# Performance work log

Measured on AMD Instinct MI355X. Metric: run time of the kernel, lower is better.

The kernel has to match this reference:

```python
import jax, jax.numpy as jnp
import numpy as np

N = 50000          # site nodes
L = 32             # max URL token length
E = 64             # embed_size
H = 128            # hidden_size
E_SIM = 800000     # edges per relation in blocks
E_SUB = 200000     # 'sim' edges classified at the end
NEG = 0.01         # LeakyReLU negative slope

def leaky(x):
    return jnp.where(x >= 0, x, NEG * x)

def lstm_final(x, mask, Wih, Whh, b, reverse):
    # x: [N, L, E], mask: [N, L] bool. Returns packed-sequence final hidden [N, E].
    if reverse:
        x = x[:, ::-1, :]
        mask = mask[:, ::-1]
    h0 = jnp.zeros((x.shape[0], Whh.shape[1]), x.dtype)
    def step(carry, inp):
        h, c = carry
        xt, mt = inp
        g = xt @ Wih.T + h @ Whh.T + b
        i, f, gg, o = jnp.split(g, 4, axis=-1)  # PyTorch gate order i,f,g,o
        cn = jax.nn.sigmoid(f) * c + jax.nn.sigmoid(i) * jnp.tanh(gg)
        hn = jax.nn.sigmoid(o) * jnp.tanh(cn)
        m = mt[:, None]
        return (jnp.where(m, hn, h), jnp.where(m, cn, c)), None
    (h, _), _ = jax.lax.scan(step, (h0, h0), (x.transpose(1, 0, 2), mask.T))
    return h

def graph_conv(h, src, dst, W, b):
    # DGL GraphConv, norm='both': D_dst^{-1/2} A D_src^{-1/2} h W + b  (degrees clamped to >=1)
    n = h.shape[0]
    ones = jnp.ones(src.shape[0], h.dtype)
    out_deg = jnp.clip(jax.ops.segment_sum(ones, src, num_segments=n), 1.0)
    in_deg = jnp.clip(jax.ops.segment_sum(ones, dst, num_segments=n), 1.0)
    feat = h * jax.lax.rsqrt(out_deg)[:, None]
    if W.shape[0] > W.shape[1]:
        feat = feat @ W  # project before gather/scatter when in_dim > out_dim (as DGL does)
        rst = jax.ops.segment_sum(feat[src], dst, num_segments=n)
    else:
        rst = jax.ops.segment_sum(feat[src], dst, num_segments=n) @ W
    return rst * jax.lax.rsqrt(in_deg)[:, None] + b

def setup_inputs():
    key = jax.random.key(0)
    ks = iter(jax.random.split(key, 64))
    def nrm(shape, scale=0.05):
        return jax.random.normal(next(ks), shape, dtype=jnp.float32) * scale
    inp = {}
    inp["inputs_s"] = jax.random.randint(next(ks), (N, L), 0, 128)
    lengths = jax.random.randint(next(ks), (N,), 1, L + 1)
    inp["inputs_sm"] = (jnp.arange(L)[None, :] < lengths[:, None]).astype(jnp.int32)
    inp["inputs_c"] = jax.random.randint(next(ks), (N, 1), 0, 101)
    inp["inputs_co"] = jax.random.randint(next(ks), (N, 1), 0, 92)
    inp["inputs_sl"] = jax.random.randint(next(ks), (N, 1), 0, 6)
    for name, m in [("sim_src", E_SIM), ("sim_dst", E_SIM), ("user_src", E_SIM),
                    ("user_dst", E_SIM), ("esub_src", E_SUB), ("esub_dst", E_SUB)]:
        inp[name] = jax.random.randint(next(ks), (m,), 0, N)
    inp["emb_url"] = nrm((128, E)); inp["emb_cat"] = nrm((101, E))
    inp["emb_country"] = nrm((92, E)); inp["emb_sl"] = nrm((6, E))
    for d in ("f", "b"):
        inp["Wih_" + d] = nrm((4 * E, E)); inp["Whh_" + d] = nrm((4 * E, E))
        inp["b_" + d] = nrm((4 * E,))  # b_ih + b_hh folded into one bias
    inp["fc_W"] = nrm((E, 2 * E)); inp["fc_b"] = nrm((E,))
    for i, din in enumerate([4 * E, H]):
        for rel in ("sim", "user"):
            inp["gcn%d_%s_W" % (i, rel)] = nrm((din, H))
            inp["gcn%d_%s_b" % (i, rel)] = nrm((H,))
    inp["cls_W1"] = nrm((H, 2 * H)); inp["cls_b1"] = nrm((H,))
    inp["bn_g"] = jnp.ones((H,), jnp.float32); inp["bn_b"] = jnp.zeros((H,), jnp.float32)
    inp["cls_W2"] = nrm((2, H)); inp["cls_b2"] = nrm((2,))
    return inp

def reference(inputs_s, inputs_sm, inputs_c, inputs_co, inputs_sl,
              sim_src, sim_dst, user_src, user_dst, esub_src, esub_dst,
              emb_url, emb_cat, emb_country, emb_sl,
              Wih_f, Whh_f, b_f, Wih_b, Whh_b, b_b, fc_W, fc_b,
              gcn0_sim_W, gcn0_sim_b, gcn0_user_W, gcn0_user_b,
              gcn1_sim_W, gcn1_sim_b, gcn1_user_W, gcn1_user_b,
              cls_W1, cls_b1, bn_g, bn_b, cls_W2, cls_b2):
    mask = inputs_sm.astype(bool)
    x = emb_url[inputs_s]                                # [N, L, E]
    hf = lstm_final(x, mask, Wih_f, Whh_f, b_f, False)   # h_n[0]
    hb = lstm_final(x, mask, Wih_b, Whh_b, b_b, True)    # h_n[1]
    h_url = leaky(jnp.concatenate([hf, hb], -1) @ fc_W.T + fc_b)  # dropout = identity (eval)
    h = jnp.concatenate([h_url, emb_cat[inputs_c[:, 0]],
                         emb_country[inputs_co[:, 0]], emb_sl[inputs_sl[:, 0]]], -1)  # [N, 4E]
    layers = [(gcn0_sim_W, gcn0_sim_b, gcn0_user_W, gcn0_user_b),
              (gcn1_sim_W, gcn1_sim_b, gcn1_user_W, gcn1_user_b)]
    for Ws, bs, Wu, bu in layers:  # HeteroGraphConv aggregate='sum'
        h = leaky(graph_conv(h, sim_src, sim_dst, Ws, bs)
                  + graph_conv(h, user_src, user_dst, Wu, bu))
    feat = jnp.concatenate([h[esub_src], h[esub_dst]], -1)  # [E_SUB, 2H]
    z = feat @ cls_W1.T + cls_b1
    z = (z - z.mean(0)) * jax.lax.rsqrt(z.var(0) + 1e-5) * bn_g + bn_b  # BatchNorm1d (batch stats)
    z = jnp.maximum(z, 0.0)
    return z @ cls_W2.T + cls_b2
```

## Files before the change

### kernel.cpp

```cpp
#include <hip/hip_runtime.h>
#include <hip/hip_bf16.h>
#include <stdint.h>

#define N_NODES 50000
#define SEQ_L   32
#define NE_BIG  800000
#define NE_SUB  200000
#define DSTRIDE 64

typedef __hip_bfloat16 bf16;
typedef unsigned short u16;
typedef _Float16 f16;
typedef _Float16 v8h __attribute__((ext_vector_type(8)));
typedef float v4f __attribute__((ext_vector_type(4)));

__device__ __forceinline__ float b2f(bf16 x) { return __bfloat162float(x); }
__device__ __forceinline__ float leakyf(float v) { return v >= 0.f ? v : 0.01f * v; }
__device__ __forceinline__ u16 f2h_bits(float x) { f16 h = (f16)x; u16 b; __builtin_memcpy(&b, &h, 2); return b; }
__device__ __forceinline__ float h2f(u16 b) { f16 h; __builtin_memcpy(&h, &b, 2); return (float)h; }
__device__ __forceinline__ uint pack2h(float a, float b) { return (uint)f2h_bits(a) | ((uint)f2h_bits(b) << 16); }

__device__ __forceinline__ float ldf(const void* p, int i, int isbf) {
  return isbf ? b2f(((const bf16*)p)[i]) : ((const float*)p)[i];
}

__device__ __forceinline__ int detect_isbf(const u16* __restrict__ u) {
  __shared__ int insane;
  if (threadIdx.x == 0) insane = 0;
  __syncthreads();
  int expo = (u[threadIdx.x * 2] >> 7) & 0xFF;
  if (expo >= 147) atomicAdd(&insane, 1);
  __syncthreads();
  return insane == 0;
}

struct PrepArgs {
  const void* Whh_f; const void* Whh_b; const void* fc_W; const void* cls_W1;
  const void* g0sW; const void* g0uW; const void* g1sW; const void* g1uW;
  const void* emb_cat; const void* emb_country; const void* emb_sl;
  const void* fc_b; const void* cls_b1; const void* g0sb; const void* g0ub;
  const void* g1sb; const void* g1ub; const void* bn_g; const void* bn_b;
  const void* cls_W2; const void* cls_b2;
  const void* emb_url; const void* Wih_f; const void* b_f; const void* Wih_b; const void* b_b;
  f16* Whh_h; u16* Bfc; u16* BW1; u16* Bg0; u16* Bg1;
  u16* embc_h; u16* embco_h; u16* embs_h;
  float* fcb; float* b1; float* g0sbP; float* g0ubP; float* g1sbP; float* g1ubP;
  float* bngP; float* bnbP; float* W2P; float* b2P;
  int* cnt4; int* cnt33; int* cur33; float* bnsums; int* dflag;
  float* Xperm;
};

__global__ __launch_bounds__(256) void prep_mega_kernel(PrepArgs A) {
  const int b = blockIdx.x;
  const int t = threadIdx.x;
  const int isbf = detect_isbf((const u16*)A.emb_url);
  auto cpy = [&](const void* s, float* d, int n, int boff) {
    int i = (b - boff) * 256 + t;
    if (i < n) d[i] = ldf(s, i, isbf);
  };
  auto cvh = [&](const void* s, u16* d, int n, int boff) {
    int i = (b - boff) * 256 + t;
    if (i < n) d[i] = f2h_bits(ldf(s, i, isbf));
  };
  auto trh = [&](const void* s, u16* d, int R, int C, int KOFF, int boff) {
    int i = (b - boff) * 256 + t;
    if (i < R * C) { int r = i / C, c = i % C; d[c * 256 + KOFF + r] = f2h_bits(ldf(s, i, isbf)); }
  };
  if      (b <   64) cvh(A.Whh_f, (u16*)A.Whh_h, 16384, 0);
  else if (b <  128) cvh(A.Whh_b, (u16*)(A.Whh_h + 16384), 16384, 64);
  else if (b <  160) cvh(A.fc_W, A.Bfc, 8192, 128);
  else if (b <  288) cvh(A.cls_W1, A.BW1, 32768, 160);
  else if (b <  416) trh(A.g0sW, A.Bg0, 256, 128, 0, 288);
  else if (b <  544) trh(A.g0uW, A.Bg0 + 128 * 256, 256, 128, 0, 416);
  else if (b <  608) trh(A.g1sW, A.Bg1, 128, 128, 0, 544);
  else if (b <  672) trh(A.g1uW, A.Bg1, 128, 128, 128, 608);
  else if (b <  698) cvh(A.emb_cat, A.embc_h, 6464, 672);
  else if (b <  721) cvh(A.emb_country, A.embco_h, 5888, 698);
  else if (b <  723) cvh(A.emb_sl, A.embs_h, 384, 721);
  else if (b <  724) cpy(A.fc_b, A.fcb, 64, 723);
  else if (b <  725) cpy(A.cls_b1, A.b1, 128, 724);
  else if (b <  726) cpy(A.g0sb, A.g0sbP, 128, 725);
  else if (b <  727) cpy(A.g0ub, A.g0ubP, 128, 726);
  else if (b <  728) cpy(A.g1sb, A.g1sbP, 128, 727);
  else if (b <  729) cpy(A.g1ub, A.g1ubP, 128, 728);
  else if (b <  730) cpy(A.bn_g, A.bngP, 128, 729);
  else if (b <  731) cpy(A.bn_b, A.bnbP, 128, 730);
  else if (b <  732) cpy(A.cls_W2, A.W2P, 256, 731);
  else if (b <  733) cpy(A.cls_b2, A.b2P, 2, 732);
  else if (b < 1515) {
    int i = (b - 733) * 256 + t;
    if (i < 4 * N_NODES) A.cnt4[i] = 0;
  } else if (b < 1516) {
    if (t < 64) { A.cnt33[t] = 0; A.cur33[t] = 0; }
    A.bnsums[t] = 0.f;
    if (t == 0) A.dflag[0] = isbf;
  } else {
    int bb = b - 1516;
    int dir = bb >> 7;
    int v = bb & 127;
    const void* Wih = dir ? A.Wih_b : A.Wih_f;
    const void* bias = dir ? A.b_b : A.b_f;
    __shared__ float embL[64];
    if (t < 64) embL[t] = ldf(A.emb_url, v * 64 + t, isbf);
    __syncthreads();
    float acc = ldf(bias, t, isbf);
#pragma unroll 8
    for (int j = 0; j < 64; ++j) acc += embL[j] * ldf(Wih, t * 64 + j, isbf);
    int g = t >> 6, unit = t & 63;
    A.Xperm[(size_t)dir * 128 * 256 + v * 256 + unit * 4 + g] = acc;
  }
}
#define PREP_BLOCKS 1772

__global__ __launch_bounds__(256) void graph_build_kernel(
    const int* __restrict__ sm, int* __restrict__ lens, int* __restrict__ cnt33,
    const int* __restrict__ s0, const int* __restrict__ d0,
    const int* __restrict__ s1, const int* __restrict__ d1,
    int* __restrict__ cnt4, int* __restrict__ col0, int* __restrict__ col1)
{
  const int b = blockIdx.x, t = threadIdx.x;
  const int NBL = (N_NODES + 255) / 256;
  const int NBE = (NE_BIG + 255) / 256;
  if (b < NBL) {
    int i = b * 256 + t;
    if (i >= N_NODES) return;
    int len = 0;
#pragma unroll
    for (int tt = 0; tt < SEQ_L; ++tt) len += sm[i * SEQ_L + tt];
    lens[i] = len;
    atomicAdd(&cnt33[len], 1);
  } else {
    int rel = (b - NBL) / NBE;
    int e = ((b - NBL) % NBE) * 256 + t;
    if (e >= NE_BIG) return;
    const int* s = rel ? s1 : s0;
    const int* d = rel ? d1 : d0;
    int* col = rel ? col1 : col0;
    int* base = cnt4 + (size_t)rel * 2 * N_NODES;
    int sv = s[e], dv = d[e];
    atomicAdd(&base[sv], 1);
    int p = atomicAdd(&base[N_NODES + dv], 1);
    if (p < DSTRIDE) col[(size_t)dv * DSTRIDE + p] = sv;
  }
}
#define GB_BLOCKS (196 + 2 * 3125)

__global__ __launch_bounds__(256) void permfill_rsq_kernel(
    const int* __restrict__ lens, const int* __restrict__ cnt33, int* __restrict__ cur33,
    int* __restrict__ perm,
    const int* __restrict__ cnt4, float* __restrict__ rsq4)
{
  const int b = blockIdx.x, t = threadIdx.x;
  const int NBL = (N_NODES + 255) / 256;
  if (b < NBL) {
    int i = b * 256 + t;
    if (i >= N_NODES) return;
    int len = lens[i];
    int base = 0;
    for (int l = len + 1; l <= SEQ_L; ++l) base += cnt33[l];
    int p = atomicAdd(&cur33[len], 1);
    perm[base + p] = i;
  } else {
    int i = (b - NBL) * 256 + t;
    if (i >= 4 * N_NODES) return;
    int c = cnt4[i]; if (c < 1) c = 1;
    rsq4[i] = __builtin_amdgcn_rsqf((float)c);
  }
}
#define PR_BLOCKS (196 + 782)

__global__ __launch_bounds__(256, 3) void lstm_mfma_kernel(
    const int* __restrict__ perm, const int* __restrict__ lens,
    const int* __restrict__ toksg,
    const float* __restrict__ Xperm,
    const f16* __restrict__ Whh_h,
    u16* __restrict__ hcat_h,
    int nnodes)
{
  __shared__ __align__(16) f16 H[2][64 * 72];
  __shared__ int toksL[2][64];
  __shared__ int permL[64];
  __shared__ int lensL[64];
  __shared__ int smax;
  const int tid = threadIdx.x;
  const int w = tid >> 6;
  const int lane = tid & 63;
  const int quad = lane >> 4;
  const int lid = lane & 15;
  const int dir = blockIdx.y;

  if (tid < 64) {
    int gid = blockIdx.x * 64 + tid;
    int node = -1, len = 0;
    if (gid < nnodes) { node = perm[gid]; len = lens[node]; }
    permL[tid] = node; lensL[tid] = len;
  }
  if (tid == 0) smax = 0;
  for (int i = tid; i < 64 * 72; i += 256) { H[0][i] = (f16)0.f; H[1][i] = (f16)0.f; }
  __syncthreads();
  if (tid < 64 && lensL[tid] > 0) atomicMax(&smax, lensL[tid]);
  __syncthreads();
  const int tmax = smax;

  const f16* Wd = Whh_h + (size_t)dir * 256 * 64;
  v8h Bf[4][2];
#pragma unroll
  for (int g = 0; g < 4; ++g)
#pragma unroll
    for (int kf = 0; kf < 2; ++kf)
      Bf[g][kf] = *(const v8h*)(Wd + (g * 64 + w * 16 + lid) * 64 + kf * 32 + quad * 8);

  int lenv[16];
#pragma unroll
  for (int mt = 0; mt < 4; ++mt)
#pragma unroll
    for (int r = 0; r < 4; ++r) lenv[mt * 4 + r] = lensL[mt * 16 + quad * 4 + r];

  float creg[16];
  f16 hreg[16];
#pragma unroll
  for (int i = 0; i < 16; ++i) { creg[i] = 0.f; hreg[i] = (f16)0.f; }

  const float* Xp = Xperm + (size_t)dir * 128 * 256;

  if (tid < 64) {
    int len = lensL[tid];
    int tok = 0;
    if (len > 0) tok = toksg[(size_t)permL[tid] * SEQ_L + (dir ? (len - 1) : 0)];
    toksL[0][tid] = tok;
  }
  __syncthreads();

  for (int step = 0; step < tmax; ++step) {
    const int rb = step & 1, wb = rb ^ 1;
#pragma unroll
    for (int mt = 0; mt < 4; ++mt) {
      float4 xr[4];
#pragma unroll
      for (int r = 0; r < 4; ++r) {
        int nd = mt * 16 + quad * 4 + r;
        xr[r] = *(const float4*)(Xp + (size_t)toksL[rb][nd] * 256 + (w * 16 + lid) * 4);
      }
      const f16* hb = &H[rb][0];
      int arow = (mt * 16 + lid) * 72 + quad * 8;
      v8h a0 = *(const v8h*)(hb + arow);
      v8h a1 = *(const v8h*)(hb + arow + 32);
      v4f acc[4];
#pragma unroll
      for (int g = 0; g < 4; ++g) {
        v4f a = {0.f, 0.f, 0.f, 0.f};
        a = __builtin_amdgcn_mfma_f32_16x16x32_f16(a0, Bf[g][0], a, 0, 0, 0);
        a = __builtin_amdgcn_mfma_f32_16x16x32_f16(a1, Bf[g][1], a, 0, 0, 0);
        acc[g] = a;
      }
#pragma unroll
      for (int r = 0; r < 4; ++r) {
        int idx = mt * 4 + r;
        int nd = mt * 16 + quad * 4 + r;
        bool act = step < lenv[idx];
        float gi = acc[0][r] + xr[r].x;
        float gf = acc[1][r] + xr[r].y;
        float gG = acc[2][r] + xr[r].z;
        float go = acc[3][r] + xr[r].w;
        float A = __expf(-gi);
        float B = __expf(-gf);
        float C = __expf(-go);
        float D = __expf(2.f * fminf(gG, 15.f));
        float sf = __builtin_amdgcn_rcpf(1.f + B);
        float sitg = (D - 1.f) * __builtin_amdgcn_rcpf((1.f + A) * (D + 1.f));
        float cn = sf * creg[idx] + sitg;
        float E = __expf(2.f * fminf(cn, 15.f));
        float hn = (E - 1.f) * __builtin_amdgcn_rcpf((1.f + C) * (E + 1.f));
        if (act) { creg[idx] = cn; hreg[idx] = (f16)hn; }
        H[wb][nd * 72 + w * 16 + lid] = hreg[idx];
      }
    }
    if (tid < 64 && step + 1 < tmax) {
      int len = lensL[tid];
      int tok = 0;
      if (step + 1 < len) {
        int t = dir ? (len - 2 - step) : (step + 1);
        tok = toksg[(size_t)permL[tid] * SEQ_L + t];
      }
      toksL[wb][tid] = tok;
    }
    __syncthreads();
  }
#pragma unroll
  for (int mt = 0; mt < 4; ++mt)
#pragma unroll
    for (int r = 0; r < 4; ++r) {
      int nd = mt * 16 + quad * 4 + r;
      int gnode = permL[nd];
      if (gnode >= 0) {
        u16 bits; f16 hv = hreg[mt * 4 + r]; __builtin_memcpy(&bits, &hv, 2);
        hcat_h[(size_t)gnode * 128 + dir * 64 + w * 16 + lid] = bits;
      }
    }
}

template<int K, int COLS, int AMODE, bool LEAKY, int OHS, bool EMB, bool BNS>
__global__ __launch_bounds__(256) void mfma_gemm(
    const u16* __restrict__ Ah,
    const int* __restrict__ esrc, const int* __restrict__ edst, const u16* __restrict__ Fh,
    const u16* __restrict__ B,
    const float* __restrict__ bias, const float* __restrict__ bias2,
    const float* __restrict__ rs0, const float* __restrict__ rs1,
    u16* __restrict__ outh0, u16* __restrict__ outh1,
    const int* __restrict__ ic, const int* __restrict__ ico, const int* __restrict__ isl,
    const u16* __restrict__ ech, const u16* __restrict__ ecoh, const u16* __restrict__ eslh,
    float* __restrict__ bnsums,
    int nrows)
{
  constexpr int AST = K + 8;
  constexpr int ABYTES = 64 * AST * 2;
  constexpr int EBYTES = 64 * 129 * 4;
  constexpr int SBYTES = (ABYTES > EBYTES) ? ABYTES : EBYTES;
  __shared__ __align__(16) char smem[SBYTES];
  u16* As = (u16*)smem;
  float* Es = (float*)smem;
  __shared__ int idxL[128];
  __shared__ float bnred[BNS ? 512 : 1];

  const int tid = threadIdx.x;
  const int w = tid >> 6;
  const int lane = tid & 63;
  const int quad = lane >> 4;
  const int lid = lane & 15;
  const int r0 = blockIdx.x * 64;

  if (AMODE == 2) {
    if (tid < 64) {
      int row = r0 + tid;
      idxL[tid] = (row < nrows) ? esrc[row] : -1;
      idxL[64 + tid] = (row < nrows) ? edst[row] : -1;
    }
    __syncthreads();
    for (int idx = tid; idx < 64 * (K / 8); idx += 256) {
      int rn = idx / (K / 8), seg = idx % (K / 8);
      int half = seg >> 4, k8 = seg & 15;
      int base = idxL[half * 64 + rn];
      uint4 v = {0u, 0u, 0u, 0u};
      if (base >= 0) v = *(const uint4*)(Fh + (size_t)base * 128 + k8 * 8);
      *(uint4*)(As + rn * AST + seg * 8) = v;
    }
  } else {
    for (int idx = tid; idx < 64 * (K / 8); idx += 256) {
      int rn = idx / (K / 8), c8 = idx % (K / 8);
      int row = r0 + rn;
      uint4 v = {0u, 0u, 0u, 0u};
      if (row < nrows) v = *(const uint4*)(Ah + (size_t)row * K + c8 * 8);
      *(uint4*)(As + rn * AST + c8 * 8) = v;
    }
  }
  __syncthreads();

  constexpr int NT = COLS / 16;
  v4f acc[NT];
#pragma unroll
  for (int i = 0; i < NT; ++i) acc[i] = (v4f){0.f, 0.f, 0.f, 0.f};

  for (int kb = 0; kb < K / 32; ++kb) {
    v8h a = *(const v8h*)((const f16*)As + (w * 16 + lid) * AST + kb * 32 + quad * 8);
#pragma unroll
    for (int ct = 0; ct < NT; ++ct) {
      v8h b = *(const v8h*)((const f16*)B + (size_t)(ct * 16 + lid) * K + kb * 32 + quad * 8);
      acc[ct] = __builtin_amdgcn_mfma_f32_16x16x32_f16(a, b, acc[ct], 0, 0, 0);
    }
  }

  constexpr int NH = (COLS > 128) ? 2 : 1;
  constexpr int CH = COLS / NH;
  float bs = 0.f, bs2 = 0.f;
#pragma unroll
  for (int h = 0; h < NH; ++h) {
    __syncthreads();
#pragma unroll
    for (int ct = 0; ct < CH / 16; ++ct) {
      int ctg = h * (CH / 16) + ct;
#pragma unroll
      for (int r = 0; r < 4; ++r)
        Es[(w * 16 + quad * 4 + r) * 129 + ct * 16 + lid] = acc[ctg][r];
    }
    __syncthreads();
    for (int idx = tid; idx < 64 * CH; idx += 256) {
      int rn = idx / CH, c = idx % CH;
      int row = r0 + rn;
      float v = 0.f;
      if (row < nrows) {
        v = Es[rn * 129 + c];
        if (bias) v += bias[h * CH + c];
        if (bias2) v += bias2[h * CH + c];
        if (LEAKY) v = leakyf(v);
        const float* rs = (h == 0) ? rs0 : rs1;
        if (rs) v *= rs[row];
        u16* oh = (h == 0) ? outh0 : outh1;
        oh[(size_t)row * OHS + c] = f2h_bits(v);
      }
      if (BNS) { bs += v; bs2 += v * v; }
    }
  }
  if (BNS) {
    bnred[tid] = bs;
    bnred[256 + tid] = bs2;
    __syncthreads();
    if (tid < 128) {
      atomicAdd(&bnsums[tid], bnred[tid] + bnred[tid + 128]);
      atomicAdd(&bnsums[128 + tid], bnred[256 + tid] + bnred[384 + tid]);
    }
  }
  if (EMB) {
    for (int idx = tid; idx < 64 * 192; idx += 256) {
      int rn = idx / 192, j = idx % 192;
      int row = r0 + rn;
      if (row >= nrows) continue;
      u16 v;
      if (j < 64)       v = ech [ic [row] * 64 + j];
      else if (j < 128) v = ecoh[ico[row] * 64 + (j - 64)];
      else              v = eslh[isl[row] * 64 + (j - 128)];
      outh0[(size_t)row * OHS + 64 + j] = v;
    }
  }
}

__global__ __launch_bounds__(256) void gather_merge0_kernel(
    const int* __restrict__ colS, const int* __restrict__ cntS, const u16* __restrict__ Ps,
    const int* __restrict__ colU, const int* __restrict__ cntU, const u16* __restrict__ Pu,
    const float* __restrict__ rsS, const float* __restrict__ rsU,
    const float* __restrict__ bS, const float* __restrict__ bU,
    u16* __restrict__ outh, int nnodes)
{
  int wave = threadIdx.x >> 6;
  int lane = threadIdx.x & 63;
  int node = __builtin_amdgcn_readfirstlane(blockIdx.x * 4 + wave);
  if (node >= nnodes) return;
  const uint* PS2 = (const uint*)Ps;
  const uint* PU2 = (const uint*)Pu;
  float2 aS = make_float2(0.f, 0.f), aU = make_float2(0.f, 0.f);
  {
    const int* col = colS + (size_t)node * DSTRIDE;
    int cnt = min(cntS[node], DSTRIDE);
    int e = 0;
    for (; e + 4 <= cnt; e += 4) {
      uint v0 = PS2[(size_t)col[e] * 64 + lane];
      uint v1 = PS2[(size_t)col[e + 1] * 64 + lane];
      uint v2 = PS2[(size_t)col[e + 2] * 64 + lane];
      uint v3 = PS2[(size_t)col[e + 3] * 64 + lane];
      aS.x += h2f((u16)v0) + h2f((u16)v1) + h2f((u16)v2) + h2f((u16)v3);
      aS.y += h2f((u16)(v0 >> 16)) + h2f((u16)(v1 >> 16)) + h2f((u16)(v2 >> 16)) + h2f((u16)(v3 >> 16));
    }
    for (; e < cnt; ++e) {
      uint v = PS2[(size_t)col[e] * 64 + lane];
      aS.x += h2f((u16)v); aS.y += h2f((u16)(v >> 16));
    }
  }
  {
    const int* col = colU + (size_t)node * DSTRIDE;
    int cnt = min(cntU[node], DSTRIDE);
    int e = 0;
    for (; e + 4 <= cnt; e += 4) {
      uint v0 = PU2[(size_t)col[e] * 64 + lane];
      uint v1 = PU2[(size_t)col[e + 1] * 64 + lane];
      uint v2 = PU2[(size_t)col[e + 2] * 64 + lane];
      uint v3 = PU2[(size_t)col[e + 3] * 64 + lane];
      aU.x += h2f((u16)v0) + h2f((u16)v1) + h2f((u16)v2) + h2f((u16)v3);
      aU.y += h2f((u16)(v0 >> 16)) + h2f((u16)(v1 >> 16)) + h2f((u16)(v2 >> 16)) + h2f((u16)(v3 >> 16));
    }
    for (; e < cnt; ++e) {
      uint v = PU2[(size_t)col[e] * 64 + lane];
      aU.x += h2f((u16)v); aU.y += h2f((u16)(v >> 16));
    }
  }
  float rS = rsS[node], rU = rsU[node];
  float2 bsv = ((const float2*)bS)[lane];
  float2 buv = ((const float2*)bU)[lane];
  float o0 = leakyf(aS.x * rS + bsv.x + aU.x * rU + buv.x);
  float o1 = leakyf(aS.y * rS + bsv.y + aU.y * rU + buv.y);
  ((uint*)outh)[(size_t)node * 64 + lane] = pack2h(o0, o1);
}

__global__ __launch_bounds__(256) void gather_cat1_kernel(
    const int* __restrict__ colS, const int* __restrict__ cntS,
    const int* __restrict__ colU, const int* __restrict__ cntU,
    const u16* __restrict__ Fh,
    const float* __restrict__ rsoutS, const float* __restrict__ rsoutU,
    const float* __restrict__ rsinS, const float* __restrict__ rsinU,
    u16* __restrict__ Acat, int nnodes)
{
  int wave = threadIdx.x >> 6;
  int lane = threadIdx.x & 63;
  int node = __builtin_amdgcn_readfirstlane(blockIdx.x * 4 + wave);
  if (node >= nnodes) return;
  const uint* F2 = (const uint*)Fh;
  float2 aS = make_float2(0.f, 0.f), aU = make_float2(0.f, 0.f);
  {
    const int* col = colS + (size_t)node * DSTRIDE;
    int cnt = min(cntS[node], DSTRIDE);
    int e = 0;
    for (; e + 2 <= cnt; e += 2) {
      int s0 = col[e], s1 = col[e + 1];
      float c0 = rsoutS[s0], c1 = rsoutS[s1];
      uint v0 = F2[(size_t)s0 * 64 + lane];
      uint v1 = F2[(size_t)s1 * 64 + lane];
      aS.x += c0 * h2f((u16)v0) + c1 * h2f((u16)v1);
      aS.y += c0 * h2f((u16)(v0 >> 16)) + c1 * h2f((u16)(v1 >> 16));
    }
    for (; e < cnt; ++e) {
      int s = col[e]; float c = rsoutS[s];
      uint v = F2[(size_t)s * 64 + lane];
      aS.x += c * h2f((u16)v); aS.y += c * h2f((u16)(v >> 16));
    }
  }
  {
    const int* col = colU + (size_t)node * DSTRIDE;
    int cnt = min(cntU[node], DSTRIDE);
    int e = 0;
    for (; e + 2 <= cnt; e += 2) {
      int s0 = col[e], s1 = col[e + 1];
      float c0 = rsoutU[s0], c1 = rsoutU[s1];
      uint v0 = F2[(size_t)s0 * 64 + lane];
      uint v1 = F2[(size_t)s1 * 64 + lane];
      aU.x += c0 * h2f((u16)v0) + c1 * h2f((u16)v1);
      aU.y += c0 * h2f((u16)(v0 >> 16)) + c1 * h2f((u16)(v1 >> 16));
    }
    for (; e < cnt; ++e) {
      int s = col[e]; float c = rsoutU[s];
      uint v = F2[(size_t)s * 64 + lane];
      aU.x += c * h2f((u16)v); aU.y += c * h2f((u16)(v >> 16));
    }
  }
  float rs = rsinS[node], ru = rsinU[node];
  ((uint*)Acat)[(size_t)node * 128 + lane] = pack2h(aS.x * rs, aS.y * rs);
  ((uint*)Acat)[(size_t)node * 128 + 64 + lane] = pack2h(aU.x * ru, aU.y * ru);
}

__global__ __launch_bounds__(256) void out_kernel(
    const u16* __restrict__ zh, const float* __restrict__ bnsums,
    const float* __restrict__ g, const float* __restrict__ bb, float M,
    const float* __restrict__ W2, const float* __restrict__ b2,
    void* __restrict__ out, int Mi, const int* __restrict__ flag)
{
  __shared__ float lds[128 * 65];
  __shared__ float red[64 * 8];
  __shared__ float ssL[256];
  const int tid = threadIdx.x;
  const int n = tid & 63;
  const int q = __builtin_amdgcn_readfirstlane(tid >> 6);
  const int r0 = blockIdx.x * 64;
  if (tid < 128) {
    float mean = bnsums[tid] / M;
    float var = bnsums[128 + tid] / M - mean * mean;
    float sc = g[tid] * __builtin_amdgcn_rsqf(var + 1e-5f);
    ssL[tid] = sc;
    ssL[128 + tid] = bb[tid] - mean * sc;
  }
  for (int idx = tid; idx < 64 * 128; idx += 256) {
    int rn = idx >> 7, j = idx & 127;
    int row = r0 + rn;
    lds[j * 65 + rn] = (row < Mi) ? h2f(zh[(size_t)row * 128 + j]) : 0.f;
  }
  __syncthreads();
  float a0 = 0.f, a1 = 0.f;
#pragma unroll 8
  for (int jj = 0; jj < 32; ++jj) {
    int j = q * 32 + jj;
    float y = lds[j * 65 + n] * ssL[j] + ssL[128 + j];
    y = y > 0.f ? y : 0.f;
    a0 += y * W2[j];
    a1 += y * W2[128 + j];
  }
  red[n * 8 + q * 2 + 0] = a0;
  red[n * 8 + q * 2 + 1] = a1;
  __syncthreads();
  if (q == 0 && (r0 + n) < Mi) {
    float o0 = red[n * 8] + red[n * 8 + 2] + red[n * 8 + 4] + red[n * 8 + 6] + b2[0];
    float o1 = red[n * 8 + 1] + red[n * 8 + 3] + red[n * 8 + 5] + red[n * 8 + 7] + b2[1];
    size_t oi = (size_t)(r0 + n) * 2;
    if (*flag) {
      ((bf16*)out)[oi + 0] = __float2bfloat16(o0);
      ((bf16*)out)[oi + 1] = __float2bfloat16(o1);
    } else {
      ((float*)out)[oi + 0] = o0;
      ((float*)out)[oi + 1] = o1;
    }
  }
}

extern "C" void kernel_launch(void* const* d_in, const int* in_sizes, int n_in,
                              void* d_out, int out_size, void* d_ws, size_t ws_size,
                              hipStream_t stream) {
  (void)in_sizes; (void)n_in; (void)out_size; (void)ws_size;
  const int N = N_NODES;
  const int* inputs_s  = (const int*)d_in[0];
  const int* inputs_sm = (const int*)d_in[1];
  const int* inputs_c  = (const int*)d_in[2];
  const int* inputs_co = (const int*)d_in[3];
  const int* inputs_sl = (const int*)d_in[4];
  const int* sim_src   = (const int*)d_in[5];
  const int* sim_dst   = (const int*)d_in[6];
  const int* user_src  = (const int*)d_in[7];
  const int* user_dst  = (const int*)d_in[8];
  const int* esub_src  = (const int*)d_in[9];
  const int* esub_dst  = (const int*)d_in[10];

  char* base = (char*)d_ws;
  size_t off = 0;
  auto alloc = [&](size_t bytes) -> char* {
    char* p = base + off;
    off += (bytes + 255) & ~(size_t)255;
    return p;
  };
  int* dflag    = (int*)alloc(256);
  f16* Whh_h    = (f16*)alloc(2 * 256 * 64 * 2);
  float* Xperm  = (float*)alloc(2 * 128 * 256 * 4);
  u16* Bfc      = (u16*)alloc(64 * 128 * 2);
  u16* BW1      = (u16*)alloc(128 * 256 * 2);
  u16* Bg0      = (u16*)alloc(256 * 256 * 2);
  u16* Bg1      = (u16*)alloc(128 * 256 * 2);
  u16* P_embc_h = (u16*)alloc(6464 * 2);
  u16* P_embco_h= (u16*)alloc(5888 * 2);
  u16* P_embs_h = (u16*)alloc(384 * 2);
  float* P_fcb  = (float*)alloc(64 * 4);
  float* P_b1   = (float*)alloc(128 * 4);
  float* P_g0sb = (float*)alloc(128 * 4);
  float* P_g0ub = (float*)alloc(128 * 4);
  float* P_g1sb = (float*)alloc(128 * 4);
  float* P_g1ub = (float*)alloc(128 * 4);
  float* P_bng  = (float*)alloc(128 * 4);
  float* P_bnb  = (float*)alloc(128 * 4);
  float* P_W2   = (float*)alloc(256 * 4);
  float* P_b2   = (float*)alloc(2 * 4);
  int* lens     = (int*)alloc((size_t)N * 4);
  int* cnt33    = (int*)alloc(64 * 4);
  int* cur33    = (int*)alloc(64 * 4);
  int* perm     = (int*)alloc((size_t)N * 4);
  int* cnt4     = (int*)alloc((size_t)4 * N * 4);
  float* rsq4   = (float*)alloc((size_t)4 * N * 4);
  float* bnsums = (float*)alloc(256 * 4);
  char* bufA = alloc((size_t)N * 256 * 4);
  char* bufB = alloc((size_t)N * 256 * 2);
  char* bufC = alloc((size_t)N * 256 * 2);
  char* bufE = alloc((size_t)N * 128 * 2);
  u16* h_h    = (u16*)bufA;
  u16* zh     = (u16*)bufA;
  int* col_sim = (int*)(bufA + (size_t)N * 256 * 2);
  int* col_usr = (int*)(bufA + (size_t)N * 256 * 2 + (size_t)N * DSTRIDE * 4);
  u16* hcat_h = (u16*)bufB;
  u16* h1_h   = (u16*)bufB;
  u16* Ps_h   = (u16*)bufC;
  u16* Pu_h   = Ps_h + (size_t)N * 128;
  u16* Acat   = (u16*)bufC;
  u16* F_h    = (u16*)bufE;

  const int NB64 = (N + 63) / 64;
  const int NBZ  = (NE_SUB + 63) / 64;

  PrepArgs PA;
  PA.Whh_f = d_in[16]; PA.Whh_b = d_in[19]; PA.fc_W = d_in[21]; PA.cls_W1 = d_in[31];
  PA.g0sW = d_in[23]; PA.g0uW = d_in[25]; PA.g1sW = d_in[27]; PA.g1uW = d_in[29];
  PA.emb_cat = d_in[12]; PA.emb_country = d_in[13]; PA.emb_sl = d_in[14];
  PA.fc_b = d_in[22]; PA.cls_b1 = d_in[32]; PA.g0sb = d_in[24]; PA.g0ub = d_in[26];
  PA.g1sb = d_in[28]; PA.g1ub = d_in[30]; PA.bn_g = d_in[33]; PA.bn_b = d_in[34];
  PA.cls_W2 = d_in[35]; PA.cls_b2 = d_in[36];
  PA.emb_url = d_in[11]; PA.Wih_f = d_in[15]; PA.b_f = d_in[17]; PA.Wih_b = d_in[18]; PA.b_b = d_in[20];
  PA.Whh_h = Whh_h; PA.Bfc = Bfc; PA.BW1 = BW1; PA.Bg0 = Bg0; PA.Bg1 = Bg1;
  PA.embc_h = P_embc_h; PA.embco_h = P_embco_h; PA.embs_h = P_embs_h;
  PA.fcb = P_fcb; PA.b1 = P_b1; PA.g0sbP = P_g0sb; PA.g0ubP = P_g0ub; PA.g1sbP = P_g1sb; PA.g1ubP = P_g1ub;
  PA.bngP = P_bng; PA.bnbP = P_bnb; PA.W2P = P_W2; PA.b2P = P_b2;
  PA.cnt4 = cnt4; PA.cnt33 = cnt33; PA.cur33 = cur33; PA.bnsums = bnsums; PA.dflag = dflag;
  PA.Xperm = Xperm;
  prep_mega_kernel<<<PREP_BLOCKS, 256, 0, stream>>>(PA);

  graph_build_kernel<<<GB_BLOCKS, 256, 0, stream>>>(inputs_sm, lens, cnt33,
                                                    sim_src, sim_dst, user_src, user_dst,
                                                    cnt4, col_sim, col_usr);

  permfill_rsq_kernel<<<PR_BLOCKS, 256, 0, stream>>>(lens, cnt33, cur33, perm, cnt4, rsq4);

  lstm_mfma_kernel<<<dim3(NB64, 2), 256, 0, stream>>>(perm, lens, inputs_s, Xperm, Whh_h, hcat_h, N);

  mfma_gemm<128, 64, 1, true, 256, true, false><<<NB64, 256, 0, stream>>>(
      hcat_h, nullptr, nullptr, nullptr, Bfc, P_fcb, nullptr, nullptr, nullptr,
      h_h, nullptr, inputs_c, inputs_co, inputs_sl, P_embc_h, P_embco_h, P_embs_h, nullptr, N);

  mfma_gemm<256, 256, 1, false, 128, false, false><<<NB64, 256, 0, stream>>>(
      h_h, nullptr, nullptr, nullptr, Bg0, nullptr, nullptr, rsq4, rsq4 + 2 * N,
      Ps_h, Pu_h, nullptr, nullptr, nullptr, nullptr, nullptr, nullptr, nullptr, N);

  gather_merge0_kernel<<<(N + 3) / 4, 256, 0, stream>>>(col_sim, cnt4 + N, Ps_h,
                                                        col_usr, cnt4 + 3 * N, Pu_h,
                                                        rsq4 + N, rsq4 + 3 * N, P_g0sb, P_g0ub, h1_h, N);

  gather_cat1_kernel<<<(N + 3) / 4, 256, 0, stream>>>(col_sim, cnt4 + N, col_usr, cnt4 + 3 * N, h1_h,
                                                      rsq4, rsq4 + 2 * N, rsq4 + N, rsq4 + 3 * N, Acat, N);

  mfma_gemm<256, 128, 1, true, 128, false, false><<<NB64, 256, 0, stream>>>(
      Acat, nullptr, nullptr, nullptr, Bg1, P_g1sb, P_g1ub, nullptr, nullptr,
      F_h, nullptr, nullptr, nullptr, nullptr, nullptr, nullptr, nullptr, nullptr, N);

  mfma_gemm<256, 128, 2, false, 128, false, true><<<NBZ, 256, 0, stream>>>(
      nullptr, esub_src, esub_dst, F_h, BW1, P_b1, nullptr, nullptr, nullptr,
      zh, nullptr, nullptr, nullptr, nullptr, nullptr, nullptr, nullptr, bnsums, NE_SUB);

  out_kernel<<<NBZ, 256, 0, stream>>>(zh, bnsums, P_bng, P_bnb, (float)NE_SUB,
                                      P_W2, P_b2, d_out, NE_SUB, dflag);
}
```

Before: 1.163 ms.

## Merge prep and graph-build kernels, zero counters via memset, raise LSTM occupancy

Counter and BN-sum buffers are now one contiguous region cleared with hipMemsetAsync instead of by blocks inside the prep kernel. The weight-prep work, the sequence-length counting and the edge degree/CSR build now run in a single launch, which removes one kernel boundary and lets independent work overlap. The LSTM kernel's launch bound goes from 3 to 4 blocks per SM, which may force register spills. The memset adds its own small stream operation.

```diff
diff --git a/kernel.cpp b/kernel.cpp
--- a/kernel.cpp
+++ b/kernel.cpp
@@ -46,13 +46,44 @@
   u16* embc_h; u16* embco_h; u16* embs_h;
   float* fcb; float* b1; float* g0sbP; float* g0ubP; float* g1sbP; float* g1ubP;
   float* bngP; float* bnbP; float* W2P; float* b2P;
-  int* cnt4; int* cnt33; int* cur33; float* bnsums; int* dflag;
+  int* dflag;
   float* Xperm;
+  const int* sm; int* lens; int* cnt33;
+  const int* s0; const int* d0; const int* s1; const int* d1;
+  int* cnt4; int* col0; int* col1;
 };
 
-__global__ __launch_bounds__(256) void prep_mega_kernel(PrepArgs A) {
+__global__ __launch_bounds__(256) void prep_graph_kernel(PrepArgs A) {
   const int b = blockIdx.x;
   const int t = threadIdx.x;
+  const int NBL = (N_NODES + 255) / 256;
+  const int NBE = (NE_BIG + 255) / 256;
+
+  if (b >= 1186) {
+    int rel = (b - 1186) / NBE;
+    int e = ((b - 1186) % NBE) * 256 + t;
+    if (e >= NE_BIG) return;
+    const int* s = rel ? A.s1 : A.s0;
+    const int* d = rel ? A.d1 : A.d0;
+    int* col = rel ? A.col1 : A.col0;
+    int* base = A.cnt4 + (size_t)rel * 2 * N_NODES;
+    int sv = s[e], dv = d[e];
+    atomicAdd(&base[sv], 1);
+    int p = atomicAdd(&base[N_NODES + dv], 1);
+    if (p < DSTRIDE) col[(size_t)dv * DSTRIDE + p] = sv;
+    return;
+  }
+  if (b >= 990) {
+    int i = (b - 990) * 256 + t;
+    if (i >= N_NODES) return;
+    int len = 0;
+#pragma unroll
+    for (int tt = 0; tt < SEQ_L; ++tt) len += A.sm[i * SEQ_L + tt];
+    A.lens[i] = len;
+    atomicAdd(&A.cnt33[len], 1);
+    return;
+  }
+
   const int isbf = detect_isbf((const u16*)A.emb_url);
   auto cpy = [&](const void* s, float* d, int n, int boff) {
     int i = (b - boff) * 256 + t;
@@ -86,16 +117,9 @@
   else if (b <  730) cpy(A.bn_g, A.bngP, 128, 729);
   else if (b <  731) cpy(A.bn_b, A.bnbP, 128, 730);
   else if (b <  732) cpy(A.cls_W2, A.W2P, 256, 731);
-  else if (b <  733) cpy(A.cls_b2, A.b2P, 2, 732);
-  else if (b < 1515) {
-    int i = (b - 733) * 256 + t;
-    if (i < 4 * N_NODES) A.cnt4[i] = 0;
-  } else if (b < 1516) {
-    if (t < 64) { A.cnt33[t] = 0; A.cur33[t] = 0; }
-    A.bnsums[t] = 0.f;
-    if (t == 0) A.dflag[0] = isbf;
-  } else {
-    int bb = b - 1516;
+  else if (b <  733) { cpy(A.cls_b2, A.b2P, 2, 732); if (t == 0) A.dflag[0] = isbf; }
+  else if (b <  989) {
+    int bb = b - 733;
     int dir = bb >> 7;
     int v = bb & 127;
     const void* Wih = dir ? A.Wih_b : A.Wih_f;
@@ -110,40 +134,7 @@
     A.Xperm[(size_t)dir * 128 * 256 + v * 256 + unit * 4 + g] = acc;
   }
 }
-#define PREP_BLOCKS 1772
-
-__global__ __launch_bounds__(256) void graph_build_kernel(
-    const int* __restrict__ sm, int* __restrict__ lens, int* __restrict__ cnt33,
-    const int* __restrict__ s0, const int* __restrict__ d0,
-    const int* __restrict__ s1, const int* __restrict__ d1,
-    int* __restrict__ cnt4, int* __restrict__ col0, int* __restrict__ col1)
-{
-  const int b = blockIdx.x, t = threadIdx.x;
-  const int NBL = (N_NODES + 255) / 256;
-  const int NBE = (NE_BIG + 255) / 256;
-  if (b < NBL) {
-    int i = b * 256 + t;
-    if (i >= N_NODES) return;
-    int len = 0;
-#pragma unroll
-    for (int tt = 0; tt < SEQ_L; ++tt) len += sm[i * SEQ_L + tt];
-    lens[i] = len;
-    atomicAdd(&cnt33[len], 1);
-  } else {
-    int rel = (b - NBL) / NBE;
-    int e = ((b - NBL) % NBE) * 256 + t;
-    if (e >= NE_BIG) return;
-    const int* s = rel ? s1 : s0;
-    const int* d = rel ? d1 : d0;
-    int* col = rel ? col1 : col0;
-    int* base = cnt4 + (size_t)rel * 2 * N_NODES;
-    int sv = s[e], dv = d[e];
-    atomicAdd(&base[sv], 1);
-    int p = atomicAdd(&base[N_NODES + dv], 1);
-    if (p < DSTRIDE) col[(size_t)dv * DSTRIDE + p] = sv;
-  }
-}
-#define GB_BLOCKS (196 + 2 * 3125)
+#define PG_BLOCKS (1186 + 2 * 3125)
 
 __global__ __launch_bounds__(256) void permfill_rsq_kernel(
     const int* __restrict__ lens, const int* __restrict__ cnt33, int* __restrict__ cur33,
@@ -169,7 +160,7 @@
 }
 #define PR_BLOCKS (196 + 782)
 
-__global__ __launch_bounds__(256, 3) void lstm_mfma_kernel(
+__global__ __launch_bounds__(256, 4) void lstm_mfma_kernel(
     const int* __restrict__ perm, const int* __restrict__ lens,
     const int* __restrict__ toksg,
     const float* __restrict__ Xperm,
@@ -631,18 +622,20 @@
   float* P_W2   = (float*)alloc(256 * 4);
   float* P_b2   = (float*)alloc(2 * 4);
   int* lens     = (int*)alloc((size_t)N * 4);
-  int* cnt33    = (int*)alloc(64 * 4);
-  int* cur33    = (int*)alloc(64 * 4);
   int* perm     = (int*)alloc((size_t)N * 4);
-  int* cnt4     = (int*)alloc((size_t)4 * N * 4);
   float* rsq4   = (float*)alloc((size_t)4 * N * 4);
-  float* bnsums = (float*)alloc(256 * 4);
+  char* zbase   = alloc((size_t)4 * N * 4 + 3 * 256 + 1024);
+  int* cnt4     = (int*)zbase;
+  int* cnt33    = (int*)(zbase + (size_t)4 * N * 4);
+  int* cur33    = cnt33 + 64;
+  float* bnsums = (float*)(zbase + (size_t)4 * N * 4 + 512);
+  const size_t zbytes = (size_t)4 * N * 4 + 3 * 256 + 1024;
   char* bufA = alloc((size_t)N * 256 * 4);
   char* bufB = alloc((size_t)N * 256 * 2);
   char* bufC = alloc((size_t)N * 256 * 2);
   char* bufE = alloc((size_t)N * 128 * 2);
-  u16* h_h    = (u16*)bufA;
-  u16* zh     = (u16*)bufA;
+  u16* h_h     = (u16*)bufA;
+  u16* zh      = (u16*)bufA;
   int* col_sim = (int*)(bufA + (size_t)N * 256 * 2);
   int* col_usr = (int*)(bufA + (size_t)N * 256 * 2 + (size_t)N * DSTRIDE * 4);
   u16* hcat_h = (u16*)bufB;
@@ -654,6 +647,8 @@
 
   const int NB64 = (N + 63) / 64;
   const int NBZ  = (NE_SUB + 63) / 64;
+
+  hipMemsetAsync(zbase, 0, zbytes, stream);
 
   PrepArgs PA;
   PA.Whh_f = d_in[16]; PA.Whh_b = d_in[19]; PA.fc_W = d_in[21]; PA.cls_W1 = d_in[31];
@@ -667,13 +662,11 @@
   PA.embc_h = P_embc_h; PA.embco_h = P_embco_h; PA.embs_h = P_embs_h;
   PA.fcb = P_fcb; PA.b1 = P_b1; PA.g0sbP = P_g0sb; PA.g0ubP = P_g0ub; PA.g1sbP = P_g1sb; PA.g1ubP = P_g1ub;
   PA.bngP = P_bng; PA.bnbP = P_bnb; PA.W2P = P_W2; PA.b2P = P_b2;
-  PA.cnt4 = cnt4; PA.cnt33 = cnt33; PA.cur33 = cur33; PA.bnsums = bnsums; PA.dflag = dflag;
-  PA.Xperm = Xperm;
-  prep_mega_kernel<<<PREP_BLOCKS, 256, 0, stream>>>(PA);
-
-  graph_build_kernel<<<GB_BLOCKS, 256, 0, stream>>>(inputs_sm, lens, cnt33,
-                                                    sim_src, sim_dst, user_src, user_dst,
-                                                    cnt4, col_sim, col_usr);
+  PA.dflag = dflag; PA.Xperm = Xperm;
+  PA.sm = inputs_sm; PA.lens = lens; PA.cnt33 = cnt33;
+  PA.s0 = sim_src; PA.d0 = sim_dst; PA.s1 = user_src; PA.d1 = user_dst;
+  PA.cnt4 = cnt4; PA.col0 = col_sim; PA.col1 = col_usr;
+  prep_graph_kernel<<<PG_BLOCKS, 256, 0, stream>>>(PA);
 
   permfill_rsq_kernel<<<PR_BLOCKS, 256, 0, stream>>>(lens, cnt33, cur33, perm, cnt4, rsq4);
 
```

Result: faster. 1.130 ms (-2.9%).
